# Kernel tuning notes

Measured on AMD Instinct MI355X. Metric: run time of the kernel, lower is better.

Reference implementation:

```python
import jax, jax.numpy as jnp
import numpy as np

B, T, C, H = 4, 2048, 1024, 16
D = C // H  # head_dim = 64


def setup_inputs() -> dict:
    key = jax.random.key(0)
    k1, k2, k3 = jax.random.split(key, 3)
    x = jax.random.normal(k1, (B, T, C), dtype=jnp.float32)
    w_attn = jax.random.normal(k2, (C, 3 * C), dtype=jnp.float32) * (1.0 / np.sqrt(C))
    b_attn = jnp.zeros((3 * C,), dtype=jnp.float32)
    w_proj = jax.random.normal(k3, (C, C), dtype=jnp.float32) * (1.0 / np.sqrt(C))
    b_proj = jnp.zeros((C,), dtype=jnp.float32)
    return {"x": x, "w_attn": w_attn, "b_attn": b_attn, "w_proj": w_proj, "b_proj": b_proj}


def reference(x, w_attn, b_attn, w_proj, b_proj):
    Bx, Tx, Cx = x.shape
    qkv = x @ w_attn + b_attn                      # (B, T, 3C)
    q, k, v = jnp.split(qkv, 3, axis=2)
    # (B, T, C) -> (B, H, T, D)
    q = q.reshape(Bx, Tx, H, D).transpose(0, 2, 1, 3)
    k = k.reshape(Bx, Tx, H, D).transpose(0, 2, 1, 3)
    v = v.reshape(Bx, Tx, H, D).transpose(0, 2, 1, 3)
    scores = jnp.einsum('bhqd,bhkd->bhqk', q, k) / jnp.sqrt(jnp.float32(D))
    causal = jnp.tril(jnp.ones((Tx, Tx), dtype=bool))
    scores = jnp.where(causal[None, None], scores, jnp.float32(-jnp.inf))
    probs = jax.nn.softmax(scores, axis=-1)
    out = jnp.einsum('bhqk,bhkd->bhqd', probs, v)  # (B, H, T, D)
    out = out.transpose(0, 2, 1, 3).reshape(Bx, Tx, Cx)
    return out @ w_proj + b_proj
```

## Files before the change

### kernel.cpp

```cpp
#include <hip/hip_runtime.h>

#define AS1 __attribute__((address_space(1)))
#define AS3 __attribute__((address_space(3)))

using bf16x8  = __attribute__((ext_vector_type(8))) __bf16;
using floatx4 = __attribute__((ext_vector_type(4))) float;

__device__ inline ushort f2b(float f) {
    unsigned u = __builtin_bit_cast(unsigned, f);
    u = (u + 0x7fffu + ((u >> 16) & 1u)) >> 16;
    return (ushort)u;
}

__global__ void k_conv(const float* __restrict__ in, ushort* __restrict__ out, int n) {
    int i = (blockIdx.x * 256 + threadIdx.x) * 4;
    if (i < n) {
        float4 v = *(const float4*)(in + i);
        ushort4 o;
        o.x = f2b(v.x); o.y = f2b(v.y); o.z = f2b(v.z); o.w = f2b(v.w);
        *(ushort4*)(out + i) = o;
    }
}

__global__ void k_transpose(const float* __restrict__ in, ushort* __restrict__ out, int R, int Ncol) {
    __shared__ float tile[32][33];
    int tx = threadIdx.x & 31, ty = threadIdx.x >> 5;
    int c0 = blockIdx.x * 32, r0 = blockIdx.y * 32;
    for (int i = 0; i < 32; i += 8)
        tile[ty + i][tx] = in[(size_t)(r0 + ty + i) * Ncol + c0 + tx];
    __syncthreads();
    for (int i = 0; i < 32; i += 8)
        out[(size_t)(c0 + ty + i) * R + r0 + tx] = f2b(tile[tx][ty + i]);
}

template<bool BF16_OUT>
__global__ __launch_bounds__(256, 2) void k_gemm_bt(
    const ushort* __restrict__ A, const ushort* __restrict__ Bt,
    const float* __restrict__ bias, void* __restrict__ outv,
    int M, int N, int K)
{
    __shared__ __align__(16) ushort As[128 * 32];
    __shared__ __align__(16) ushort Bs[128 * 32];
    int tid = threadIdx.x;
    int m0 = blockIdx.y * 128, n0 = blockIdx.x * 128;
    int lane = tid & 63;
    int wm = (tid >> 7) * 64;
    int wn = ((tid >> 6) & 1) * 64;
    int lr = lane & 15;
    int quad = lane >> 4;
    int lk = quad * 8;

    floatx4 acc[4][4] = {};
    const ushort* ag = A  + (size_t)(m0 + (tid >> 2)) * K + (tid & 3) * 8;
    const ushort* bg = Bt + (size_t)(n0 + (tid >> 2)) * K + (tid & 3) * 8;
    ushort* asd = &As[tid * 8];
    ushort* bsd = &Bs[tid * 8];

    for (int kt = 0; kt < K; kt += 32) {
        __builtin_amdgcn_global_load_lds((const AS1 unsigned int*)(ag + kt),                    (AS3 unsigned int*)(asd),        16, 0, 0);
        __builtin_amdgcn_global_load_lds((const AS1 unsigned int*)(ag + kt + (size_t)64 * K),   (AS3 unsigned int*)(asd + 2048), 16, 0, 0);
        __builtin_amdgcn_global_load_lds((const AS1 unsigned int*)(bg + kt),                    (AS3 unsigned int*)(bsd),        16, 0, 0);
        __builtin_amdgcn_global_load_lds((const AS1 unsigned int*)(bg + kt + (size_t)64 * K),   (AS3 unsigned int*)(bsd + 2048), 16, 0, 0);
        asm volatile("s_waitcnt vmcnt(0)" ::: "memory");
        __syncthreads();
        bf16x8 af[4], bf[4];
        #pragma unroll
        for (int i = 0; i < 4; ++i) af[i] = *(const bf16x8*)&As[(wm + 16 * i + lr) * 32 + lk];
        #pragma unroll
        for (int j = 0; j < 4; ++j) bf[j] = *(const bf16x8*)&Bs[(wn + 16 * j + lr) * 32 + lk];
        #pragma unroll
        for (int i = 0; i < 4; ++i)
            #pragma unroll
            for (int j = 0; j < 4; ++j)
                acc[i][j] = __builtin_amdgcn_mfma_f32_16x16x32_bf16(af[i], bf[j], acc[i][j], 0, 0, 0);
        __syncthreads();
    }

    #pragma unroll
    for (int j = 0; j < 4; ++j) {
        int col = n0 + wn + 16 * j + lr;
        float bv = bias[col];
        #pragma unroll
        for (int i = 0; i < 4; ++i) {
            int row = m0 + wm + 16 * i + quad * 4;
            #pragma unroll
            for (int r = 0; r < 4; ++r) {
                float v = acc[i][j][r] + bv;
                if (BF16_OUT) ((ushort*)outv)[(size_t)(row + r) * N + col] = f2b(v);
                else          ((float*)outv)[(size_t)(row + r) * N + col] = v;
            }
        }
    }
}

__global__ __launch_bounds__(512, 4) void k_attn(const ushort* __restrict__ qkv, ushort* __restrict__ out)
{
    constexpr int T = 2048, S3 = 3072, C = 1024;
    __shared__ __align__(16) ushort Ks[64 * 64];
    __shared__ __align__(16) ushort Vt[64 * 72];
    __shared__ __align__(16) ushort Ps[8 * 16 * 72];
    int tid = threadIdx.x;
    int lane = tid & 63, wave = tid >> 6;
    int lr = lane & 15, quad = lane >> 4, lk = quad * 8;
    int bh = blockIdx.y;
    int b = bh >> 4, h = bh & 15;
    size_t base = (size_t)b * T * S3;
    const ushort* kg0 = qkv + base + C + h * 64;
    const ushort* vg0 = qkv + base + 2 * C + h * 64;
    ushort* psw = &Ps[wave * 16 * 72];
    const float SC = 0.125f * 1.44269504f;

    int skey = tid >> 3;
    int sg   = (tid & 7) ^ (skey & 7);
    ushort* ksdst = &Ks[tid * 8];

    int qts[2] = { (int)blockIdx.x, 15 - (int)blockIdx.x };
    for (int ti = 0; ti < 2; ++ti) {
        int qt = qts[ti];
        int qrow = qt * 128 + wave * 16;
        const ushort* qp = qkv + base + (size_t)(qrow + lr) * S3 + h * 64;
        bf16x8 aq0 = *(const bf16x8*)(qp + lk);
        bf16x8 aq1 = *(const bf16x8*)(qp + 32 + lk);
        floatx4 o[4] = {};
        float lsum[4] = {0.f, 0.f, 0.f, 0.f};
        int ktmax = 2 * qt + 1;

        for (int kt = 0; kt <= ktmax; ++kt) {
            __syncthreads();
            __builtin_amdgcn_global_load_lds(
                (const AS1 unsigned int*)(kg0 + (size_t)(kt * 64 + skey) * S3 + sg * 8),
                (AS3 unsigned int*)ksdst, 16, 0, 0);
            {
                int c = wave;
                const uint4* vp = (const uint4*)(vg0 + (size_t)(kt * 64 + lane) * S3 + c * 8);
                union { uint4 q; ushort us[8]; } own, oth;
                own.q = *vp;
                oth.q.x = (unsigned)__shfl_xor((int)own.q.x, 1);
                oth.q.y = (unsigned)__shfl_xor((int)own.q.y, 1);
                oth.q.z = (unsigned)__shfl_xor((int)own.q.z, 1);
                oth.q.w = (unsigned)__shfl_xor((int)own.q.w, 1);
                if (!(lane & 1)) {
                    #pragma unroll
                    for (int j = 0; j < 4; ++j)
                        *(unsigned*)&Vt[(c * 8 + j) * 72 + lane] =
                            (unsigned)own.us[j] | ((unsigned)oth.us[j] << 16);
                } else {
                    #pragma unroll
                    for (int j = 0; j < 4; ++j)
                        *(unsigned*)&Vt[(c * 8 + 4 + j) * 72 + (lane - 1)] =
                            (unsigned)oth.us[4 + j] | ((unsigned)own.us[4 + j] << 16);
                }
            }
            asm volatile("s_waitcnt vmcnt(0)" ::: "memory");
            __syncthreads();
            if (kt * 64 > qrow + 15) continue;

            floatx4 s[4];
            #pragma unroll
            for (int j = 0; j < 4; ++j) {
                int keyb = 16 * j + lr;
                bf16x8 bk0 = *(const bf16x8*)&Ks[keyb * 64 + (( quad      ) ^ (lr & 7)) * 8];
                bf16x8 bk1 = *(const bf16x8*)&Ks[keyb * 64 + (((4 + quad)) ^ (lr & 7)) * 8];
                floatx4 z = {};
                s[j] = __builtin_amdgcn_mfma_f32_16x16x32_bf16(aq0, bk0, z, 0, 0, 0);
                s[j] = __builtin_amdgcn_mfma_f32_16x16x32_bf16(aq1, bk1, s[j], 0, 0, 0);
            }
            int qg = qrow + quad * 4;
            #pragma unroll
            for (int r = 0; r < 4; ++r) {
                #pragma unroll
                for (int j = 0; j < 4; ++j) {
                    int keyg = kt * 64 + 16 * j + lr;
                    float v = s[j][r] * SC;
                    v = (keyg > qg + r) ? -30000.f : v;
                    float p = exp2f(v);
                    lsum[r] += p;
                    psw[(quad * 4 + r) * 72 + 16 * j + lr] = f2b(p);
                }
            }
            asm volatile("s_waitcnt lgkmcnt(0)" ::: "memory");
            bf16x8 ap0 = *(const bf16x8*)&psw[lr * 72 + lk];
            bf16x8 ap1 = *(const bf16x8*)&psw[lr * 72 + 32 + lk];
            #pragma unroll
            for (int jd = 0; jd < 4; ++jd) {
                bf16x8 bv0 = *(const bf16x8*)&Vt[(16 * jd + lr) * 72 + lk];
                bf16x8 bv1 = *(const bf16x8*)&Vt[(16 * jd + lr) * 72 + 32 + lk];
                o[jd] = __builtin_amdgcn_mfma_f32_16x16x32_bf16(ap0, bv0, o[jd], 0, 0, 0);
                o[jd] = __builtin_amdgcn_mfma_f32_16x16x32_bf16(ap1, bv1, o[jd], 0, 0, 0);
            }
        }

        #pragma unroll
        for (int r = 0; r < 4; ++r) {
            float t = lsum[r];
            t += __shfl_xor(t, 1, 16);
            t += __shfl_xor(t, 2, 16);
            t += __shfl_xor(t, 4, 16);
            t += __shfl_xor(t, 8, 16);
            float inv = 1.0f / t;
            int row = b * T + qrow + quad * 4 + r;
            #pragma unroll
            for (int jd = 0; jd < 4; ++jd)
                out[(size_t)row * C + h * 64 + 16 * jd + lr] = f2b(o[jd][r] * inv);
        }
    }
}

extern "C" void kernel_launch(void* const* d_in, const int* in_sizes, int n_in,
                              void* d_out, int out_size, void* d_ws, size_t ws_size,
                              hipStream_t stream) {
    const float* x      = (const float*)d_in[0];
    const float* w_attn = (const float*)d_in[1];
    const float* b_attn = (const float*)d_in[2];
    const float* w_proj = (const float*)d_in[3];
    const float* b_proj = (const float*)d_in[4];
    float* out = (float*)d_out;

    constexpr int Bb = 4, T = 2048, C = 1024;
    constexpr int M = Bb * T;

    ushort* xb  = (ushort*)d_ws;
    ushort* waT = xb  + (size_t)M * C;
    ushort* wpT = waT + (size_t)3 * C * C;
    ushort* qkv = wpT + (size_t)C * C;
    ushort* ao  = qkv + (size_t)M * 3 * C;

    k_conv<<<(M * C / 4 + 255) / 256, 256, 0, stream>>>(x, xb, M * C);
    k_transpose<<<dim3(3 * C / 32, C / 32), 256, 0, stream>>>(w_attn, waT, C, 3 * C);
    k_transpose<<<dim3(C / 32, C / 32), 256, 0, stream>>>(w_proj, wpT, C, C);
    k_gemm_bt<true ><<<dim3(3 * C / 128, M / 128), 256, 0, stream>>>(xb, waT, b_attn, qkv, M, 3 * C, C);
    k_attn<<<dim3(8, Bb * 16), 512, 0, stream>>>(qkv, ao);
    k_gemm_bt<false><<<dim3(C / 128, M / 128), 256, 0, stream>>>(ao, wpT, b_proj, out, M, C, C);
}
```

Before: 287.7 us.

## Emit transposed V from QKV GEMM, fold softmax scale into weights, MFMA row sums

The QKV GEMM now writes Q/K into a 2048-wide buffer and writes V directly in transposed per-head layout, so the attention kernel can load V with async global-to-LDS copies instead of shuffling and transposing it in registers. The softmax scale and log2e factor are folded into the Q weights and bias, which removes a multiply per score. Causal masking is applied only on the diagonal tile, and row sums are computed with an MFMA against a ones vector instead of per-element adds and shuffles. This trades some extra LDS traffic and bf16-rounded denominators for fewer VALU operations per tile.

```diff
diff --git a/kernel.cpp b/kernel.cpp
--- a/kernel.cpp
+++ b/kernel.cpp
@@ -6,10 +6,11 @@
 using bf16x8  = __attribute__((ext_vector_type(8))) __bf16;
 using floatx4 = __attribute__((ext_vector_type(4))) float;
 
+#define SCQ 0.18033688f
+
 __device__ inline ushort f2b(float f) {
-    unsigned u = __builtin_bit_cast(unsigned, f);
-    u = (u + 0x7fffu + ((u >> 16) & 1u)) >> 16;
-    return (ushort)u;
+    __bf16 h = (__bf16)f;
+    return __builtin_bit_cast(ushort, h);
 }
 
 __global__ void k_conv(const float* __restrict__ in, ushort* __restrict__ out, int n) {
@@ -22,21 +23,25 @@
     }
 }
 
-__global__ void k_transpose(const float* __restrict__ in, ushort* __restrict__ out, int R, int Ncol) {
+__global__ void k_transpose(const float* __restrict__ in, ushort* __restrict__ out,
+                            int R, int Ncol, float scale, int scale_cols) {
     __shared__ float tile[32][33];
     int tx = threadIdx.x & 31, ty = threadIdx.x >> 5;
     int c0 = blockIdx.x * 32, r0 = blockIdx.y * 32;
     for (int i = 0; i < 32; i += 8)
         tile[ty + i][tx] = in[(size_t)(r0 + ty + i) * Ncol + c0 + tx];
     __syncthreads();
-    for (int i = 0; i < 32; i += 8)
-        out[(size_t)(c0 + ty + i) * R + r0 + tx] = f2b(tile[tx][ty + i]);
-}
-
-template<bool BF16_OUT>
+    for (int i = 0; i < 32; i += 8) {
+        int n = c0 + ty + i;
+        float v = tile[tx][ty + i];
+        if (n < scale_cols) v *= scale;
+        out[(size_t)n * R + r0 + tx] = f2b(v);
+    }
+}
+
 __global__ __launch_bounds__(256, 2) void k_gemm_bt(
     const ushort* __restrict__ A, const ushort* __restrict__ Bt,
-    const float* __restrict__ bias, void* __restrict__ outv,
+    const float* __restrict__ bias, float* __restrict__ outv,
     int M, int N, int K)
 {
     __shared__ __align__(16) ushort As[128 * 32];
@@ -46,9 +51,7 @@
     int lane = tid & 63;
     int wm = (tid >> 7) * 64;
     int wn = ((tid >> 6) & 1) * 64;
-    int lr = lane & 15;
-    int quad = lane >> 4;
-    int lk = quad * 8;
+    int lr = lane & 15, quad = lane >> 4, lk = quad * 8;
 
     floatx4 acc[4][4] = {};
     const ushort* ag = A  + (size_t)(m0 + (tid >> 2)) * K + (tid & 3) * 8;
@@ -57,10 +60,10 @@
     ushort* bsd = &Bs[tid * 8];
 
     for (int kt = 0; kt < K; kt += 32) {
-        __builtin_amdgcn_global_load_lds((const AS1 unsigned int*)(ag + kt),                    (AS3 unsigned int*)(asd),        16, 0, 0);
-        __builtin_amdgcn_global_load_lds((const AS1 unsigned int*)(ag + kt + (size_t)64 * K),   (AS3 unsigned int*)(asd + 2048), 16, 0, 0);
-        __builtin_amdgcn_global_load_lds((const AS1 unsigned int*)(bg + kt),                    (AS3 unsigned int*)(bsd),        16, 0, 0);
-        __builtin_amdgcn_global_load_lds((const AS1 unsigned int*)(bg + kt + (size_t)64 * K),   (AS3 unsigned int*)(bsd + 2048), 16, 0, 0);
+        __builtin_amdgcn_global_load_lds((const AS1 unsigned int*)(ag + kt),                  (AS3 unsigned int*)(asd),        16, 0, 0);
+        __builtin_amdgcn_global_load_lds((const AS1 unsigned int*)(ag + kt + (size_t)64 * K), (AS3 unsigned int*)(asd + 2048), 16, 0, 0);
+        __builtin_amdgcn_global_load_lds((const AS1 unsigned int*)(bg + kt),                  (AS3 unsigned int*)(bsd),        16, 0, 0);
+        __builtin_amdgcn_global_load_lds((const AS1 unsigned int*)(bg + kt + (size_t)64 * K), (AS3 unsigned int*)(bsd + 2048), 16, 0, 0);
         asm volatile("s_waitcnt vmcnt(0)" ::: "memory");
         __syncthreads();
         bf16x8 af[4], bf[4];
@@ -84,107 +87,172 @@
         for (int i = 0; i < 4; ++i) {
             int row = m0 + wm + 16 * i + quad * 4;
             #pragma unroll
-            for (int r = 0; r < 4; ++r) {
-                float v = acc[i][j][r] + bv;
-                if (BF16_OUT) ((ushort*)outv)[(size_t)(row + r) * N + col] = f2b(v);
-                else          ((float*)outv)[(size_t)(row + r) * N + col] = v;
-            }
-        }
-    }
-}
-
-__global__ __launch_bounds__(512, 4) void k_attn(const ushort* __restrict__ qkv, ushort* __restrict__ out)
+            for (int r = 0; r < 4; ++r)
+                outv[(size_t)(row + r) * N + col] = acc[i][j][r] + bv;
+        }
+    }
+}
+
+__global__ __launch_bounds__(256, 2) void k_gemm_qkv(
+    const ushort* __restrict__ A, const ushort* __restrict__ Bt,
+    const float* __restrict__ bias, ushort* __restrict__ qkv, ushort* __restrict__ vt)
 {
-    constexpr int T = 2048, S3 = 3072, C = 1024;
+    constexpr int K = 1024;
+    __shared__ __align__(16) ushort As[128 * 32];
+    __shared__ __align__(16) ushort Bs[128 * 32];
+    int tid = threadIdx.x;
+    int m0 = blockIdx.y * 128, n0 = blockIdx.x * 128;
+    int lane = tid & 63;
+    int wm = (tid >> 7) * 64;
+    int wn = ((tid >> 6) & 1) * 64;
+    int lr = lane & 15, quad = lane >> 4, lk = quad * 8;
+
+    floatx4 acc[4][4] = {};
+    const ushort* ag = A  + (size_t)(m0 + (tid >> 2)) * K + (tid & 3) * 8;
+    const ushort* bg = Bt + (size_t)(n0 + (tid >> 2)) * K + (tid & 3) * 8;
+    ushort* asd = &As[tid * 8];
+    ushort* bsd = &Bs[tid * 8];
+
+    for (int kt = 0; kt < K; kt += 32) {
+        __builtin_amdgcn_global_load_lds((const AS1 unsigned int*)(ag + kt),                  (AS3 unsigned int*)(asd),        16, 0, 0);
+        __builtin_amdgcn_global_load_lds((const AS1 unsigned int*)(ag + kt + (size_t)64 * K), (AS3 unsigned int*)(asd + 2048), 16, 0, 0);
+        __builtin_amdgcn_global_load_lds((const AS1 unsigned int*)(bg + kt),                  (AS3 unsigned int*)(bsd),        16, 0, 0);
+        __builtin_amdgcn_global_load_lds((const AS1 unsigned int*)(bg + kt + (size_t)64 * K), (AS3 unsigned int*)(bsd + 2048), 16, 0, 0);
+        asm volatile("s_waitcnt vmcnt(0)" ::: "memory");
+        __syncthreads();
+        bf16x8 af[4], bf[4];
+        #pragma unroll
+        for (int i = 0; i < 4; ++i) af[i] = *(const bf16x8*)&As[(wm + 16 * i + lr) * 32 + lk];
+        #pragma unroll
+        for (int j = 0; j < 4; ++j) bf[j] = *(const bf16x8*)&Bs[(wn + 16 * j + lr) * 32 + lk];
+        #pragma unroll
+        for (int i = 0; i < 4; ++i)
+            #pragma unroll
+            for (int j = 0; j < 4; ++j)
+                acc[i][j] = __builtin_amdgcn_mfma_f32_16x16x32_bf16(af[i], bf[j], acc[i][j], 0, 0, 0);
+        __syncthreads();
+    }
+
+    int bb = m0 >> 11;
+    #pragma unroll
+    for (int j = 0; j < 4; ++j) {
+        int col = n0 + wn + 16 * j + lr;
+        float bv = bias[col];
+        if (col < 1024) bv *= SCQ;
+        if (col < 2048) {
+            #pragma unroll
+            for (int i = 0; i < 4; ++i) {
+                int row = m0 + wm + 16 * i + quad * 4;
+                #pragma unroll
+                for (int r = 0; r < 4; ++r)
+                    qkv[(size_t)(row + r) * 2048 + col] = f2b(acc[i][j][r] + bv);
+            }
+        } else {
+            int h = (col - 2048) >> 6, d = (col - 2048) & 63;
+            ushort* vbase = vt + ((size_t)(bb * 16 + h) * 64 + d) * 2048;
+            #pragma unroll
+            for (int i = 0; i < 4; ++i) {
+                int t0 = (m0 + wm + 16 * i + quad * 4) & 2047;
+                ushort4 pk;
+                ((ushort*)&pk)[0] = f2b(acc[i][j][0] + bv);
+                ((ushort*)&pk)[1] = f2b(acc[i][j][1] + bv);
+                ((ushort*)&pk)[2] = f2b(acc[i][j][2] + bv);
+                ((ushort*)&pk)[3] = f2b(acc[i][j][3] + bv);
+                *(ushort4*)&vbase[t0] = pk;
+            }
+        }
+    }
+}
+
+__global__ __launch_bounds__(512, 4) void k_attn(const ushort* __restrict__ qkv,
+                                                 const ushort* __restrict__ vt,
+                                                 ushort* __restrict__ out)
+{
+    constexpr int T = 2048, SQK = 2048, C = 1024;
     __shared__ __align__(16) ushort Ks[64 * 64];
-    __shared__ __align__(16) ushort Vt[64 * 72];
+    __shared__ __align__(16) ushort Vs[64 * 64];
     __shared__ __align__(16) ushort Ps[8 * 16 * 72];
     int tid = threadIdx.x;
     int lane = tid & 63, wave = tid >> 6;
     int lr = lane & 15, quad = lane >> 4, lk = quad * 8;
     int bh = blockIdx.y;
     int b = bh >> 4, h = bh & 15;
-    size_t base = (size_t)b * T * S3;
-    const ushort* kg0 = qkv + base + C + h * 64;
-    const ushort* vg0 = qkv + base + 2 * C + h * 64;
+    size_t base = (size_t)b * T * SQK;
+    const ushort* kg0 = qkv + base + 1024 + h * 64;
+    const ushort* vg0 = vt + (size_t)bh * 64 * 2048;
     ushort* psw = &Ps[wave * 16 * 72];
-    const float SC = 0.125f * 1.44269504f;
-
-    int skey = tid >> 3;
-    int sg   = (tid & 7) ^ (skey & 7);
+
+    int srow = tid >> 3;
+    int sg   = (tid & 7) ^ (srow & 7);
     ushort* ksdst = &Ks[tid * 8];
+    ushort* vsdst = &Vs[tid * 8];
+    const ushort* kgs = kg0 + (size_t)srow * SQK + sg * 8;
+    const ushort* vgs = vg0 + (size_t)srow * 2048 + sg * 8;
+
+    bf16x8 ones;
+    #pragma unroll
+    for (int i = 0; i < 8; ++i) ones[i] = (__bf16)1.0f;
+    int c0 = (quad ^ (lr & 7)) * 8;
+    int c1 = ((4 + quad) ^ (lr & 7)) * 8;
 
     int qts[2] = { (int)blockIdx.x, 15 - (int)blockIdx.x };
     for (int ti = 0; ti < 2; ++ti) {
         int qt = qts[ti];
         int qrow = qt * 128 + wave * 16;
-        const ushort* qp = qkv + base + (size_t)(qrow + lr) * S3 + h * 64;
+        int kt_d = qrow >> 6;
+        const ushort* qp = qkv + base + (size_t)(qrow + lr) * SQK + h * 64;
         bf16x8 aq0 = *(const bf16x8*)(qp + lk);
         bf16x8 aq1 = *(const bf16x8*)(qp + 32 + lk);
         floatx4 o[4] = {};
-        float lsum[4] = {0.f, 0.f, 0.f, 0.f};
+        floatx4 lacc = {};
         int ktmax = 2 * qt + 1;
 
         for (int kt = 0; kt <= ktmax; ++kt) {
             __syncthreads();
-            __builtin_amdgcn_global_load_lds(
-                (const AS1 unsigned int*)(kg0 + (size_t)(kt * 64 + skey) * S3 + sg * 8),
-                (AS3 unsigned int*)ksdst, 16, 0, 0);
-            {
-                int c = wave;
-                const uint4* vp = (const uint4*)(vg0 + (size_t)(kt * 64 + lane) * S3 + c * 8);
-                union { uint4 q; ushort us[8]; } own, oth;
-                own.q = *vp;
-                oth.q.x = (unsigned)__shfl_xor((int)own.q.x, 1);
-                oth.q.y = (unsigned)__shfl_xor((int)own.q.y, 1);
-                oth.q.z = (unsigned)__shfl_xor((int)own.q.z, 1);
-                oth.q.w = (unsigned)__shfl_xor((int)own.q.w, 1);
-                if (!(lane & 1)) {
-                    #pragma unroll
-                    for (int j = 0; j < 4; ++j)
-                        *(unsigned*)&Vt[(c * 8 + j) * 72 + lane] =
-                            (unsigned)own.us[j] | ((unsigned)oth.us[j] << 16);
-                } else {
-                    #pragma unroll
-                    for (int j = 0; j < 4; ++j)
-                        *(unsigned*)&Vt[(c * 8 + 4 + j) * 72 + (lane - 1)] =
-                            (unsigned)oth.us[4 + j] | ((unsigned)own.us[4 + j] << 16);
-                }
-            }
+            __builtin_amdgcn_global_load_lds((const AS1 unsigned int*)(kgs + (size_t)kt * 64 * SQK),
+                                             (AS3 unsigned int*)ksdst, 16, 0, 0);
+            __builtin_amdgcn_global_load_lds((const AS1 unsigned int*)(vgs + kt * 64),
+                                             (AS3 unsigned int*)vsdst, 16, 0, 0);
             asm volatile("s_waitcnt vmcnt(0)" ::: "memory");
             __syncthreads();
-            if (kt * 64 > qrow + 15) continue;
+            if (kt > kt_d) continue;
 
             floatx4 s[4];
             #pragma unroll
             for (int j = 0; j < 4; ++j) {
-                int keyb = 16 * j + lr;
-                bf16x8 bk0 = *(const bf16x8*)&Ks[keyb * 64 + (( quad      ) ^ (lr & 7)) * 8];
-                bf16x8 bk1 = *(const bf16x8*)&Ks[keyb * 64 + (((4 + quad)) ^ (lr & 7)) * 8];
+                const ushort* kr = &Ks[(16 * j + lr) * 64];
+                bf16x8 bk0 = *(const bf16x8*)(kr + c0);
+                bf16x8 bk1 = *(const bf16x8*)(kr + c1);
                 floatx4 z = {};
                 s[j] = __builtin_amdgcn_mfma_f32_16x16x32_bf16(aq0, bk0, z, 0, 0, 0);
                 s[j] = __builtin_amdgcn_mfma_f32_16x16x32_bf16(aq1, bk1, s[j], 0, 0, 0);
             }
-            int qg = qrow + quad * 4;
-            #pragma unroll
-            for (int r = 0; r < 4; ++r) {
+            if (kt == kt_d) {
+                int qg = qrow + quad * 4, kb = kt * 64;
                 #pragma unroll
-                for (int j = 0; j < 4; ++j) {
-                    int keyg = kt * 64 + 16 * j + lr;
-                    float v = s[j][r] * SC;
-                    v = (keyg > qg + r) ? -30000.f : v;
-                    float p = exp2f(v);
-                    lsum[r] += p;
-                    psw[(quad * 4 + r) * 72 + 16 * j + lr] = f2b(p);
-                }
+                for (int r = 0; r < 4; ++r)
+                    #pragma unroll
+                    for (int j = 0; j < 4; ++j) {
+                        float p = ((kb + 16 * j + lr) > (qg + r)) ? 0.f : exp2f(s[j][r]);
+                        psw[(quad * 4 + r) * 72 + 16 * j + lr] = f2b(p);
+                    }
+            } else {
+                #pragma unroll
+                for (int r = 0; r < 4; ++r)
+                    #pragma unroll
+                    for (int j = 0; j < 4; ++j)
+                        psw[(quad * 4 + r) * 72 + 16 * j + lr] = f2b(exp2f(s[j][r]));
             }
             asm volatile("s_waitcnt lgkmcnt(0)" ::: "memory");
             bf16x8 ap0 = *(const bf16x8*)&psw[lr * 72 + lk];
             bf16x8 ap1 = *(const bf16x8*)&psw[lr * 72 + 32 + lk];
+            lacc = __builtin_amdgcn_mfma_f32_16x16x32_bf16(ap0, ones, lacc, 0, 0, 0);
+            lacc = __builtin_amdgcn_mfma_f32_16x16x32_bf16(ap1, ones, lacc, 0, 0, 0);
             #pragma unroll
             for (int jd = 0; jd < 4; ++jd) {
-                bf16x8 bv0 = *(const bf16x8*)&Vt[(16 * jd + lr) * 72 + lk];
-                bf16x8 bv1 = *(const bf16x8*)&Vt[(16 * jd + lr) * 72 + 32 + lk];
+                const ushort* vr = &Vs[(16 * jd + lr) * 64];
+                bf16x8 bv0 = *(const bf16x8*)(vr + c0);
+                bf16x8 bv1 = *(const bf16x8*)(vr + c1);
                 o[jd] = __builtin_amdgcn_mfma_f32_16x16x32_bf16(ap0, bv0, o[jd], 0, 0, 0);
                 o[jd] = __builtin_amdgcn_mfma_f32_16x16x32_bf16(ap1, bv1, o[jd], 0, 0, 0);
             }
@@ -192,12 +260,7 @@
 
         #pragma unroll
         for (int r = 0; r < 4; ++r) {
-            float t = lsum[r];
-            t += __shfl_xor(t, 1, 16);
-            t += __shfl_xor(t, 2, 16);
-            t += __shfl_xor(t, 4, 16);
-            t += __shfl_xor(t, 8, 16);
-            float inv = 1.0f / t;
+            float inv = 1.0f / lacc[r];
             int row = b * T + qrow + quad * 4 + r;
             #pragma unroll
             for (int jd = 0; jd < 4; ++jd)
@@ -223,12 +286,13 @@
     ushort* waT = xb  + (size_t)M * C;
     ushort* wpT = waT + (size_t)3 * C * C;
     ushort* qkv = wpT + (size_t)C * C;
-    ushort* ao  = qkv + (size_t)M * 3 * C;
+    ushort* vt  = qkv + (size_t)M * 2 * C;
+    ushort* ao  = vt  + (size_t)64 * 64 * T;
 
     k_conv<<<(M * C / 4 + 255) / 256, 256, 0, stream>>>(x, xb, M * C);
-    k_transpose<<<dim3(3 * C / 32, C / 32), 256, 0, stream>>>(w_attn, waT, C, 3 * C);
-    k_transpose<<<dim3(C / 32, C / 32), 256, 0, stream>>>(w_proj, wpT, C, C);
-    k_gemm_bt<true ><<<dim3(3 * C / 128, M / 128), 256, 0, stream>>>(xb, waT, b_attn, qkv, M, 3 * C, C);
-    k_attn<<<dim3(8, Bb * 16), 512, 0, stream>>>(qkv, ao);
-    k_gemm_bt<false><<<dim3(C / 128, M / 128), 256, 0, stream>>>(ao, wpT, b_proj, out, M, C, C);
-}
+    k_transpose<<<dim3(3 * C / 32, C / 32), 256, 0, stream>>>(w_attn, waT, C, 3 * C, SCQ, C);
+    k_transpose<<<dim3(C / 32, C / 32), 256, 0, stream>>>(w_proj, wpT, C, C, 1.0f, 0);
+    k_gemm_qkv<<<dim3(3 * C / 128, M / 128), 256, 0, stream>>>(xb, waT, b_attn, qkv, vt);
+    k_attn<<<dim3(8, Bb * 16), 512, 0, stream>>>(qkv, vt, ao);
+    k_gemm_bt<<<dim3(C / 128, M / 128), 256, 0, stream>>>(ao, wpT, b_proj, out, M, C, C);
+}
```

After: 262.5 us. 1.1x faster.
